# Performance work log

Hardware: AMD Instinct MI355X
Metric: run time of the kernel (lower is better)

Reference implementation:

```python
import jax, jax.numpy as jnp
import numpy as np

B, C, L, E = 65536, 16, 32, 32
EPS = 1e-12

def _normalize(x, axis=-1):
    # F.normalize: x / max(||x||_2, eps)
    n = jnp.sqrt(jnp.sum(x * x, axis=axis, keepdims=True))
    return x / jnp.maximum(n, EPS)

def _linear(x, W, b):
    # torch nn.Linear: y = x @ W.T + b, W: [out, in]
    return jnp.einsum('bcl,el->bce', x, W) + b

def setup_inputs() -> dict:
    key = jax.random.key(0)
    ks = jax.random.split(key, 12)
    s_l = 1.0 / np.sqrt(L)
    s_p1 = 1.0 / np.sqrt(C * E)
    s_p2 = 1.0 / np.sqrt(C * 3)
    return {
        'embed1': jax.random.normal(ks[0], (B, C, L), jnp.float32),
        'embed2': jax.random.normal(ks[1], (B, C, L), jnp.float32),
        'qW': jax.random.uniform(ks[2], (E, L), jnp.float32, -s_l, s_l),
        'qb': jax.random.uniform(ks[3], (E,), jnp.float32, -s_l, s_l),
        'kW': jax.random.uniform(ks[4], (E, L), jnp.float32, -s_l, s_l),
        'kb': jax.random.uniform(ks[5], (E,), jnp.float32, -s_l, s_l),
        'vW': jax.random.uniform(ks[6], (E, L), jnp.float32, -s_l, s_l),
        'vb': jax.random.uniform(ks[7], (E,), jnp.float32, -s_l, s_l),
        'p1W': jax.random.uniform(ks[8], (C * 3, C * E), jnp.float32, -s_p1, s_p1),
        'p1b': jax.random.uniform(ks[9], (C * 3,), jnp.float32, -s_p1, s_p1),
        'p2W': jax.random.uniform(ks[10], (3, C * 3), jnp.float32, -s_p2, s_p2),
        'p2b': jax.random.uniform(ks[11], (3,), jnp.float32, -s_p2, s_p2),
    }

def reference(embed1, embed2, qW, qb, kW, kb, vW, vb, p1W, p1b, p2W, p2b):
    query = _linear(embed1, qW, qb) * _linear(embed2, qW, qb)   # [B,C,E]
    key_t = _linear(embed1, kW, kb) * _linear(embed2, kW, kb)   # [B,C,E]
    value = _linear(embed1, vW, vb) * _linear(embed2, vW, vb)   # [B,C,E]
    attn = jnp.einsum('bce,bde->bcd', _normalize(query), _normalize(key_t))  # [B,C,C]
    # torch F.softmax with dim=None on a 3-D tensor -> legacy dim=0 (batch axis)
    attn = jax.nn.softmax(attn, axis=0)
    # dropout(p=0.2) is identity in eval mode
    out = jnp.einsum('bcd,bce->bde', attn, value)  # attn.transpose(1,2) @ value, [B,C,E]
    h = out.reshape(out.shape[0], -1)              # [B, C*E]
    h = jax.nn.relu(h @ p1W.T + p1b) @ p2W.T + p2b  # [B, 3]
    return _normalize(h)
```

## Files before the change

### kernel.cpp

```cpp
#include <hip/hip_runtime.h>

#define B_TOT 65536
#define WS_P1W 4096
#define WS_EV  (1u << 20)

typedef float f32x4 __attribute__((ext_vector_type(4)));
typedef short s16x8 __attribute__((ext_vector_type(8)));

__device__ __forceinline__ unsigned short f2bf(float f) {
    unsigned u = __builtin_bit_cast(unsigned, f);
    u += 0x7fffu + ((u >> 16) & 1u);
    return (unsigned short)(u >> 16);
}
__device__ __forceinline__ float bf2f(unsigned short h) {
    unsigned u = ((unsigned)h) << 16;
    return __builtin_bit_cast(float, u);
}
__device__ __forceinline__ unsigned pack2(float a, float b) {
    return (unsigned)f2bf(a) | ((unsigned)f2bf(b) << 16);
}
__device__ __forceinline__ s16x8 cvt8(float4 a, float4 b) {
    s16x8 r;
    r[0] = (short)f2bf(a.x); r[1] = (short)f2bf(a.y);
    r[2] = (short)f2bf(a.z); r[3] = (short)f2bf(a.w);
    r[4] = (short)f2bf(b.x); r[5] = (short)f2bf(b.y);
    r[6] = (short)f2bf(b.z); r[7] = (short)f2bf(b.w);
    return r;
}
#define MFMA(a, b, c) __builtin_amdgcn_mfma_f32_16x16x32_bf16((a), (b), (c), 0, 0, 0)

__global__ __launch_bounds__(256) void k0_prep(const float* __restrict__ p1W,
                                               char* __restrict__ ws) {
    int idx = blockIdx.x * 256 + threadIdx.x;
    if (blockIdx.x == 0 && threadIdx.x < 256)
        ((float*)ws)[threadIdx.x] = 0.f;
    int jj   = idx & 7;
    int lane = (idx >> 3) & 63;
    int ktnt = idx >> 9;
    int kt = ktnt & 15, nt = ktnt >> 4;
    int n_lo = lane & 15, q8 = lane >> 4;
    int j  = nt * 16 + n_lo;
    int ip = kt * 32 + q8 * 8 + jj;
    int e_lo = ip >> 5, qq = (ip >> 3) & 3, hh = (ip >> 2) & 1, r = ip & 3;
    int orig = (qq * 4 + r) * 32 + (e_lo + 16 * hh);
    ((unsigned short*)(ws + WS_P1W))[idx] = f2bf(p1W[j * 512 + orig]);
}

__global__ __launch_bounds__(256) void k1_stats(
    const float* __restrict__ e1, const float* __restrict__ e2,
    const float* __restrict__ qW, const float* __restrict__ qb,
    const float* __restrict__ kW, const float* __restrict__ kb,
    const float* __restrict__ vW, const float* __restrict__ vb,
    char* __restrict__ ws) {

    const int tid = threadIdx.x;
    const int lane = tid & 63;
    const int widx = tid >> 6;
    const int col = lane & 15;
    const int quad = lane >> 4;

    __shared__ __align__(16) unsigned short qk_lds[4][2][16 * 40];
    __shared__ float Dblk[256];
    Dblk[tid] = 0.f;
    __syncthreads();

    s16x8 wq[2], wk[2], wv[2];
    float qbias[2], kbias[2], vbias[2];
    for (int h = 0; h < 2; ++h) {
        int row = col + 16 * h;
        const float4* pq = (const float4*)(qW + row * 32 + quad * 8);
        const float4* pk = (const float4*)(kW + row * 32 + quad * 8);
        const float4* pv = (const float4*)(vW + row * 32 + quad * 8);
        wq[h] = cvt8(pq[0], pq[1]);
        wk[h] = cvt8(pk[0], pk[1]);
        wv[h] = cvt8(pv[0], pv[1]);
        qbias[h] = qb[row]; kbias[h] = kb[row]; vbias[h] = vb[row];
    }

    unsigned short* qbuf = qk_lds[widx][0];
    unsigned short* kbuf = qk_lds[widx][1];
    float dacc[4] = {0.f, 0.f, 0.f, 0.f};
    char* evbase = ws + WS_EV;
    const f32x4 z = {0.f, 0.f, 0.f, 0.f};

    const int gw = blockIdx.x * 4 + widx;
    for (int i = 0; i < 16; ++i) {
        const int b = gw * 16 + i;
        const float4* x1p = (const float4*)(e1 + (size_t)b * 512 + col * 32 + quad * 8);
        const float4* x2p = (const float4*)(e2 + (size_t)b * 512 + col * 32 + quad * 8);
        float4 a0 = x1p[0], a1 = x1p[1];
        float4 b0 = x2p[0], b1 = x2p[1];
        s16x8 fx1 = cvt8(a0, a1);
        s16x8 fx2 = cvt8(b0, b1);

        f32x4 q1[2], q2[2], k1[2], k2[2], v1[2], v2[2];
        for (int h = 0; h < 2; ++h) {
            q1[h] = MFMA(fx1, wq[h], z); q2[h] = MFMA(fx2, wq[h], z);
            k1[h] = MFMA(fx1, wk[h], z); k2[h] = MFMA(fx2, wk[h], z);
            v1[h] = MFMA(fx1, wv[h], z); v2[h] = MFMA(fx2, wv[h], z);
        }
        float Qt[2][4], Kt[2][4], Vv[2][4];
        for (int h = 0; h < 2; ++h)
            for (int r = 0; r < 4; ++r) {
                Qt[h][r] = (q1[h][r] + qbias[h]) * (q2[h][r] + qbias[h]);
                Kt[h][r] = (k1[h][r] + kbias[h]) * (k2[h][r] + kbias[h]);
                Vv[h][r] = (v1[h][r] + vbias[h]) * (v2[h][r] + vbias[h]);
            }
        for (int r = 0; r < 4; ++r) {
            int w = (quad * 4 + r) * 20 + col;
            ((unsigned*)qbuf)[w] = pack2(Qt[0][r], Qt[1][r]);
            ((unsigned*)kbuf)[w] = pack2(Kt[0][r], Kt[1][r]);
        }
        s16x8 aq = *(const s16x8*)(qbuf + col * 40 + quad * 8);
        s16x8 bk = *(const s16x8*)(kbuf + col * 40 + quad * 8);
        float qv[8], kv[8], ssq = 0.f, ssk = 0.f;
        for (int j = 0; j < 8; ++j) {
            qv[j] = bf2f((unsigned short)aq[j]); ssq += qv[j] * qv[j];
            kv[j] = bf2f((unsigned short)bk[j]); ssk += kv[j] * kv[j];
        }
        ssq += __shfl_xor(ssq, 16); ssq += __shfl_xor(ssq, 32);
        ssk += __shfl_xor(ssk, 16); ssk += __shfl_xor(ssk, 32);
        float sq = 1.f / fmaxf(sqrtf(ssq), 1e-12f);
        float sk = 1.f / fmaxf(sqrtf(ssk), 1e-12f);
        for (int j = 0; j < 8; ++j) {
            aq[j] = (short)f2bf(qv[j] * sq);
            bk[j] = (short)f2bf(kv[j] * sk);
        }
        f32x4 S = MFMA(aq, bk, z);

        char* bbase = evbase + (size_t)b * 1536;
        float ex[4];
        for (int r = 0; r < 4; ++r) { ex[r] = __expf(S[r]); dacc[r] += ex[r]; }
        uint2 est; est.x = pack2(ex[0], ex[1]); est.y = pack2(ex[2], ex[3]);
        *(uint2*)(bbase + col * 32 + quad * 8) = est;
        for (int h = 0; h < 2; ++h) {
            uint2 vst;
            vst.x = pack2(Vv[h][0], Vv[h][1]);
            vst.y = pack2(Vv[h][2], Vv[h][3]);
            *(uint2*)(bbase + 512 + ((h * 16 + col) * 2 + (quad >> 1)) * 16 + (quad & 1) * 8) = vst;
        }
    }
    for (int r = 0; r < 4; ++r)
        atomicAdd(&Dblk[col * 16 + quad * 4 + r], dacc[r]);
    __syncthreads();
    atomicAdd(((float*)ws) + tid, Dblk[tid]);
}

__global__ __launch_bounds__(256) void k2_apply(
    const char* __restrict__ ws, const float* __restrict__ p1b,
    const float* __restrict__ p2W, const float* __restrict__ p2b,
    float* __restrict__ out) {

    const int tid = threadIdx.x;
    const int lane = tid & 63;
    const int widx = tid >> 6;
    const int col = lane & 15;
    const int quad = lane >> 4;
    const int qm = quad & 1;

    __shared__ __align__(16) unsigned short H[4][16 * 512];
    unsigned short* hrow = H[widx];

    const float* Dws = (const float*)ws;
    float dinv[8];
    for (int j = 0; j < 8; ++j)
        dinv[j] = 1.f / Dws[col * 16 + qm * 8 + j];

    float p2w[3][3], p1bias[3];
    for (int nt = 0; nt < 3; ++nt) {
        p1bias[nt] = p1b[col + 16 * nt];
        for (int t = 0; t < 3; ++t) p2w[nt][t] = p2W[t * 48 + col + 16 * nt];
    }
    const float pb0 = p2b[0], pb1 = p2b[1], pb2 = p2b[2];

    const char* evbase = ws + WS_EV;
    const unsigned short* p1wp = (const unsigned short*)(ws + WS_P1W);
    const int g = blockIdx.x * 4 + widx;
    const f32x4 z = {0.f, 0.f, 0.f, 0.f};
    const s16x8 zz = {0, 0, 0, 0, 0, 0, 0, 0};

#pragma unroll 4
    for (int i = 0; i < 16; ++i) {
        const int b = g * 16 + i;
        const char* bbase = evbase + (size_t)b * 1536;
        s16x8 eraw = *(const s16x8*)(bbase + col * 32 + qm * 16);
        s16x8 bf0 = *(const s16x8*)(bbase + 512 + (col * 2 + qm) * 16);
        s16x8 bf1 = *(const s16x8*)(bbase + 512 + ((16 + col) * 2 + qm) * 16);
        s16x8 afrag;
        for (int j = 0; j < 8; ++j)
            afrag[j] = (short)f2bf(bf2f((unsigned short)eraw[j]) * dinv[j]);
        if (quad >= 2) { afrag = zz; bf0 = zz; bf1 = zz; }
        f32x4 o0 = MFMA(afrag, bf0, z);
        f32x4 o1 = MFMA(afrag, bf1, z);
        s16x8 hp;
        for (int r = 0; r < 4; ++r) {
            hp[r]     = (short)f2bf(o0[r]);
            hp[4 + r] = (short)f2bf(o1[r]);
        }
        int chunk = (col * 4 + quad) ^ (i & 7);
        *(s16x8*)(hrow + i * 512 + chunk * 8) = hp;
    }

    f32x4 acc[3] = {z, z, z};
#pragma unroll 4
    for (int kt = 0; kt < 16; ++kt) {
        int chunk = (kt * 4 + quad) ^ (col & 7);
        s16x8 a = *(const s16x8*)(hrow + col * 512 + chunk * 8);
        for (int nt = 0; nt < 3; ++nt) {
            s16x8 bw = *(const s16x8*)(p1wp + ((nt * 16 + kt) * 64 + lane) * 8);
            acc[nt] = MFMA(a, bw, acc[nt]);
        }
    }

    float pp[4][3] = {};
    for (int nt = 0; nt < 3; ++nt)
        for (int r = 0; r < 4; ++r) {
            float hv = fmaxf(acc[nt][r] + p1bias[nt], 0.f);
            pp[r][0] += hv * p2w[nt][0];
            pp[r][1] += hv * p2w[nt][1];
            pp[r][2] += hv * p2w[nt][2];
        }
    for (int m = 1; m <= 8; m <<= 1)
        for (int r = 0; r < 4; ++r)
            for (int t = 0; t < 3; ++t)
                pp[r][t] += __shfl_xor(pp[r][t], m);
    for (int r = 0; r < 4; ++r) {
        float h0 = pp[r][0] + pb0, h1 = pp[r][1] + pb1, h2 = pp[r][2] + pb2;
        float inv = 1.f / fmaxf(sqrtf(h0 * h0 + h1 * h1 + h2 * h2), 1e-12f);
        if (col < 3) {
            float v = (col == 0) ? h0 : ((col == 1) ? h1 : h2);
            out[(size_t)(g * 16 + quad * 4 + r) * 3 + col] = v * inv;
        }
    }
}

extern "C" void kernel_launch(void* const* d_in, const int* in_sizes, int n_in,
                              void* d_out, int out_size, void* d_ws, size_t ws_size,
                              hipStream_t stream) {
    const float* e1  = (const float*)d_in[0];
    const float* e2  = (const float*)d_in[1];
    const float* qW  = (const float*)d_in[2];
    const float* qb  = (const float*)d_in[3];
    const float* kW  = (const float*)d_in[4];
    const float* kb  = (const float*)d_in[5];
    const float* vW  = (const float*)d_in[6];
    const float* vb  = (const float*)d_in[7];
    const float* p1W = (const float*)d_in[8];
    const float* p1b = (const float*)d_in[9];
    const float* p2W = (const float*)d_in[10];
    const float* p2b = (const float*)d_in[11];
    float* out = (float*)d_out;
    char* ws = (char*)d_ws;

    k0_prep<<<96, 256, 0, stream>>>(p1W, ws);
    k1_stats<<<1024, 256, 0, stream>>>(e1, e2, qW, qb, kW, kb, vW, vb, ws);
    k2_apply<<<1024, 256, 0, stream>>>(ws, p1b, p2W, p2b, out);
}
```

Measured before the change: 370.3 us.

## Cheapen bf16 packing, fold biases into MFMA, and spread work over more blocks

Replaces round-to-nearest-even bf16 conversion with add-0x8000 rounding and a byte permute, so packing two values costs fewer instructions. The linear biases now seed the MFMA accumulators instead of being added afterwards. k1 handles 8 batches per wave instead of 16 and launches twice as many blocks. k2 now gives each block 16 batch rows, splits the K dimension of the p1 GEMM across its four waves and reduces their partials through LDS, which cuts LDS use per block and allows more blocks in flight. The costs are slightly different rounding (ties round up rather than to even), extra barriers, and more atomics on the shared denominator.

```diff
diff --git a/kernel.cpp b/kernel.cpp
--- a/kernel.cpp
+++ b/kernel.cpp
@@ -7,25 +7,23 @@
 typedef float f32x4 __attribute__((ext_vector_type(4)));
 typedef short s16x8 __attribute__((ext_vector_type(8)));
 
-__device__ __forceinline__ unsigned short f2bf(float f) {
-    unsigned u = __builtin_bit_cast(unsigned, f);
-    u += 0x7fffu + ((u >> 16) & 1u);
-    return (unsigned short)(u >> 16);
-}
 __device__ __forceinline__ float bf2f(unsigned short h) {
     unsigned u = ((unsigned)h) << 16;
     return __builtin_bit_cast(float, u);
 }
 __device__ __forceinline__ unsigned pack2(float a, float b) {
-    return (unsigned)f2bf(a) | ((unsigned)f2bf(b) << 16);
+    unsigned ua = __builtin_bit_cast(unsigned, a) + 0x8000u;
+    unsigned ub = __builtin_bit_cast(unsigned, b) + 0x8000u;
+    return __builtin_amdgcn_perm(ub, ua, 0x07060302u);
+}
+__device__ __forceinline__ unsigned short f2bf(float f) {
+    return (unsigned short)((__builtin_bit_cast(unsigned, f) + 0x8000u) >> 16);
 }
 __device__ __forceinline__ s16x8 cvt8(float4 a, float4 b) {
-    s16x8 r;
-    r[0] = (short)f2bf(a.x); r[1] = (short)f2bf(a.y);
-    r[2] = (short)f2bf(a.z); r[3] = (short)f2bf(a.w);
-    r[4] = (short)f2bf(b.x); r[5] = (short)f2bf(b.y);
-    r[6] = (short)f2bf(b.z); r[7] = (short)f2bf(b.w);
-    return r;
+    uint4 u;
+    u.x = pack2(a.x, a.y); u.y = pack2(a.z, a.w);
+    u.z = pack2(b.x, b.y); u.w = pack2(b.z, b.w);
+    return __builtin_bit_cast(s16x8, u);
 }
 #define MFMA(a, b, c) __builtin_amdgcn_mfma_f32_16x16x32_bf16((a), (b), (c), 0, 0, 0)
 
@@ -65,7 +63,7 @@
     __syncthreads();
 
     s16x8 wq[2], wk[2], wv[2];
-    float qbias[2], kbias[2], vbias[2];
+    f32x4 cbq[2], cbk[2], cbv[2];
     for (int h = 0; h < 2; ++h) {
         int row = col + 16 * h;
         const float4* pq = (const float4*)(qW + row * 32 + quad * 8);
@@ -74,7 +72,10 @@
         wq[h] = cvt8(pq[0], pq[1]);
         wk[h] = cvt8(pk[0], pk[1]);
         wv[h] = cvt8(pv[0], pv[1]);
-        qbias[h] = qb[row]; kbias[h] = kb[row]; vbias[h] = vb[row];
+        float qv = qb[row], kv = kb[row], vv = vb[row];
+        cbq[h] = (f32x4){qv, qv, qv, qv};
+        cbk[h] = (f32x4){kv, kv, kv, kv};
+        cbv[h] = (f32x4){vv, vv, vv, vv};
     }
 
     unsigned short* qbuf = qk_lds[widx][0];
@@ -84,8 +85,8 @@
     const f32x4 z = {0.f, 0.f, 0.f, 0.f};
 
     const int gw = blockIdx.x * 4 + widx;
-    for (int i = 0; i < 16; ++i) {
-        const int b = gw * 16 + i;
+    for (int i = 0; i < 8; ++i) {
+        const int b = gw * 8 + i;
         const float4* x1p = (const float4*)(e1 + (size_t)b * 512 + col * 32 + quad * 8);
         const float4* x2p = (const float4*)(e2 + (size_t)b * 512 + col * 32 + quad * 8);
         float4 a0 = x1p[0], a1 = x1p[1];
@@ -95,16 +96,16 @@
 
         f32x4 q1[2], q2[2], k1[2], k2[2], v1[2], v2[2];
         for (int h = 0; h < 2; ++h) {
-            q1[h] = MFMA(fx1, wq[h], z); q2[h] = MFMA(fx2, wq[h], z);
-            k1[h] = MFMA(fx1, wk[h], z); k2[h] = MFMA(fx2, wk[h], z);
-            v1[h] = MFMA(fx1, wv[h], z); v2[h] = MFMA(fx2, wv[h], z);
+            q1[h] = MFMA(fx1, wq[h], cbq[h]); q2[h] = MFMA(fx2, wq[h], cbq[h]);
+            k1[h] = MFMA(fx1, wk[h], cbk[h]); k2[h] = MFMA(fx2, wk[h], cbk[h]);
+            v1[h] = MFMA(fx1, wv[h], cbv[h]); v2[h] = MFMA(fx2, wv[h], cbv[h]);
         }
         float Qt[2][4], Kt[2][4], Vv[2][4];
         for (int h = 0; h < 2; ++h)
             for (int r = 0; r < 4; ++r) {
-                Qt[h][r] = (q1[h][r] + qbias[h]) * (q2[h][r] + qbias[h]);
-                Kt[h][r] = (k1[h][r] + kbias[h]) * (k2[h][r] + kbias[h]);
-                Vv[h][r] = (v1[h][r] + vbias[h]) * (v2[h][r] + vbias[h]);
+                Qt[h][r] = q1[h][r] * q2[h][r];
+                Kt[h][r] = k1[h][r] * k2[h][r];
+                Vv[h][r] = v1[h][r] * v2[h][r];
             }
         for (int r = 0; r < 4; ++r) {
             int w = (quad * 4 + r) * 20 + col;
@@ -122,10 +123,13 @@
         ssk += __shfl_xor(ssk, 16); ssk += __shfl_xor(ssk, 32);
         float sq = 1.f / fmaxf(sqrtf(ssq), 1e-12f);
         float sk = 1.f / fmaxf(sqrtf(ssk), 1e-12f);
-        for (int j = 0; j < 8; ++j) {
-            aq[j] = (short)f2bf(qv[j] * sq);
-            bk[j] = (short)f2bf(kv[j] * sk);
-        }
+        uint4 uq, uk;
+        uq.x = pack2(qv[0] * sq, qv[1] * sq); uq.y = pack2(qv[2] * sq, qv[3] * sq);
+        uq.z = pack2(qv[4] * sq, qv[5] * sq); uq.w = pack2(qv[6] * sq, qv[7] * sq);
+        uk.x = pack2(kv[0] * sk, kv[1] * sk); uk.y = pack2(kv[2] * sk, kv[3] * sk);
+        uk.z = pack2(kv[4] * sk, kv[5] * sk); uk.w = pack2(kv[6] * sk, kv[7] * sk);
+        aq = __builtin_bit_cast(s16x8, uq);
+        bk = __builtin_bit_cast(s16x8, uk);
         f32x4 S = MFMA(aq, bk, z);
 
         char* bbase = evbase + (size_t)b * 1536;
@@ -158,78 +162,93 @@
     const int quad = lane >> 4;
     const int qm = quad & 1;
 
-    __shared__ __align__(16) unsigned short H[4][16 * 512];
-    unsigned short* hrow = H[widx];
+    __shared__ __align__(16) unsigned short Hs[16 * 512];
+    float* P = (float*)Hs;
 
     const float* Dws = (const float*)ws;
     float dinv[8];
     for (int j = 0; j < 8; ++j)
         dinv[j] = 1.f / Dws[col * 16 + qm * 8 + j];
 
-    float p2w[3][3], p1bias[3];
-    for (int nt = 0; nt < 3; ++nt) {
-        p1bias[nt] = p1b[col + 16 * nt];
-        for (int t = 0; t < 3; ++t) p2w[nt][t] = p2W[t * 48 + col + 16 * nt];
-    }
-    const float pb0 = p2b[0], pb1 = p2b[1], pb2 = p2b[2];
-
     const char* evbase = ws + WS_EV;
     const unsigned short* p1wp = (const unsigned short*)(ws + WS_P1W);
-    const int g = blockIdx.x * 4 + widx;
+    const int g = blockIdx.x;
     const f32x4 z = {0.f, 0.f, 0.f, 0.f};
     const s16x8 zz = {0, 0, 0, 0, 0, 0, 0, 0};
 
-#pragma unroll 4
-    for (int i = 0; i < 16; ++i) {
+    for (int ii = 0; ii < 4; ++ii) {
+        const int i = widx * 4 + ii;
         const int b = g * 16 + i;
         const char* bbase = evbase + (size_t)b * 1536;
         s16x8 eraw = *(const s16x8*)(bbase + col * 32 + qm * 16);
         s16x8 bf0 = *(const s16x8*)(bbase + 512 + (col * 2 + qm) * 16);
         s16x8 bf1 = *(const s16x8*)(bbase + 512 + ((16 + col) * 2 + qm) * 16);
-        s16x8 afrag;
+        float ef[8];
         for (int j = 0; j < 8; ++j)
-            afrag[j] = (short)f2bf(bf2f((unsigned short)eraw[j]) * dinv[j]);
+            ef[j] = bf2f((unsigned short)eraw[j]) * dinv[j];
+        uint4 ua;
+        ua.x = pack2(ef[0], ef[1]); ua.y = pack2(ef[2], ef[3]);
+        ua.z = pack2(ef[4], ef[5]); ua.w = pack2(ef[6], ef[7]);
+        s16x8 afrag = __builtin_bit_cast(s16x8, ua);
         if (quad >= 2) { afrag = zz; bf0 = zz; bf1 = zz; }
         f32x4 o0 = MFMA(afrag, bf0, z);
         f32x4 o1 = MFMA(afrag, bf1, z);
-        s16x8 hp;
-        for (int r = 0; r < 4; ++r) {
-            hp[r]     = (short)f2bf(o0[r]);
-            hp[4 + r] = (short)f2bf(o1[r]);
-        }
+        uint4 uh;
+        uh.x = pack2(o0[0], o0[1]); uh.y = pack2(o0[2], o0[3]);
+        uh.z = pack2(o1[0], o1[1]); uh.w = pack2(o1[2], o1[3]);
         int chunk = (col * 4 + quad) ^ (i & 7);
-        *(s16x8*)(hrow + i * 512 + chunk * 8) = hp;
-    }
+        *(uint4*)(Hs + i * 512 + chunk * 8) = uh;
+    }
+    __syncthreads();
 
     f32x4 acc[3] = {z, z, z};
-#pragma unroll 4
-    for (int kt = 0; kt < 16; ++kt) {
+    for (int t = 0; t < 4; ++t) {
+        int kt = widx * 4 + t;
         int chunk = (kt * 4 + quad) ^ (col & 7);
-        s16x8 a = *(const s16x8*)(hrow + col * 512 + chunk * 8);
+        s16x8 a = *(const s16x8*)(Hs + col * 512 + chunk * 8);
         for (int nt = 0; nt < 3; ++nt) {
             s16x8 bw = *(const s16x8*)(p1wp + ((nt * 16 + kt) * 64 + lane) * 8);
             acc[nt] = MFMA(a, bw, acc[nt]);
         }
     }
-
-    float pp[4][3] = {};
+    __syncthreads();
+
     for (int nt = 0; nt < 3; ++nt)
+        *(f32x4*)(P + (widx * 64 + lane) * 12 + nt * 4) = acc[nt];
+    __syncthreads();
+
+    if (widx == 0) {
+        f32x4 s[3] = {z, z, z};
+        for (int w = 0; w < 4; ++w)
+            for (int nt = 0; nt < 3; ++nt) {
+                f32x4 pv = *(const f32x4*)(P + (w * 64 + lane) * 12 + nt * 4);
+                s[nt] += pv;
+            }
+        float p2w[3][3], p1bias[3];
+        for (int nt = 0; nt < 3; ++nt) {
+            p1bias[nt] = p1b[col + 16 * nt];
+            for (int t = 0; t < 3; ++t) p2w[nt][t] = p2W[t * 48 + col + 16 * nt];
+        }
+        const float pb0 = p2b[0], pb1 = p2b[1], pb2 = p2b[2];
+        float pp[4][3] = {};
+        for (int nt = 0; nt < 3; ++nt)
+            for (int r = 0; r < 4; ++r) {
+                float hv = fmaxf(s[nt][r] + p1bias[nt], 0.f);
+                pp[r][0] += hv * p2w[nt][0];
+                pp[r][1] += hv * p2w[nt][1];
+                pp[r][2] += hv * p2w[nt][2];
+            }
+        for (int m = 1; m <= 8; m <<= 1)
+            for (int r = 0; r < 4; ++r)
+                for (int t = 0; t < 3; ++t)
+                    pp[r][t] += __shfl_xor(pp[r][t], m);
         for (int r = 0; r < 4; ++r) {
-            float hv = fmaxf(acc[nt][r] + p1bias[nt], 0.f);
-            pp[r][0] += hv * p2w[nt][0];
-            pp[r][1] += hv * p2w[nt][1];
-            pp[r][2] += hv * p2w[nt][2];
-        }
-    for (int m = 1; m <= 8; m <<= 1)
-        for (int r = 0; r < 4; ++r)
-            for (int t = 0; t < 3; ++t)
-                pp[r][t] += __shfl_xor(pp[r][t], m);
-    for (int r = 0; r < 4; ++r) {
-        float h0 = pp[r][0] + pb0, h1 = pp[r][1] + pb1, h2 = pp[r][2] + pb2;
-        float inv = 1.f / fmaxf(sqrtf(h0 * h0 + h1 * h1 + h2 * h2), 1e-12f);
-        if (col < 3) {
-            float v = (col == 0) ? h0 : ((col == 1) ? h1 : h2);
-            out[(size_t)(g * 16 + quad * 4 + r) * 3 + col] = v * inv;
+            float h0 = pp[r][0] + pb0, h1 = pp[r][1] + pb1, h2 = pp[r][2] + pb2;
+            float inv = 1.f / fmaxf(sqrtf(h0 * h0 + h1 * h1 + h2 * h2), 1e-12f);
+            if (col < 3) {
+                float v = (col == 0) ? h0 : ((col == 1) ? h1 : h2);
+                out[(size_t)(g * 16 + quad * 4 + r) * 3 + col] = v * inv;
+            }
         }
     }
 }
@@ -253,6 +272,6 @@
     char* ws = (char*)d_ws;
 
     k0_prep<<<96, 256, 0, stream>>>(p1W, ws);
-    k1_stats<<<1024, 256, 0, stream>>>(e1, e2, qW, qb, kW, kb, vW, vb, ws);
-    k2_apply<<<1024, 256, 0, stream>>>(ws, p1b, p2W, p2b, out);
-}
+    k1_stats<<<2048, 256, 0, stream>>>(e1, e2, qW, qb, kW, kb, vW, vb, ws);
+    k2_apply<<<4096, 256, 0, stream>>>(ws, p1b, p2W, p2b, out);
+}
```

New measurement: 342.2 us. -7.6%, faster.
